# Performance work log

Hardware: AMD Instinct MI355X
Metric: run time of the kernel (lower is better)

The kernel has to match this reference:

```python
import jax, jax.numpy as jnp
import numpy as np

NUM_GROUP = 512
GROUP_SIZE = 32


def setup_inputs() -> dict:
    key = jax.random.key(0)
    pts = jax.random.normal(key, (8, 8192, 6), dtype=jnp.float32)
    return {"pts": pts}


def _fps(xyz, num_group):
    """Farthest point sampling. xyz: (B, N, 3) -> indices (B, G)."""
    B, N, _ = xyz.shape

    def body(carry, _):
        dist, far = carry  # dist: (B, N) running min sq-dist to chosen set; far: (B,)
        centroid = jnp.take_along_axis(xyz, far[:, None, None], axis=1)  # (B, 1, 3)
        d = jnp.sum((xyz - centroid) ** 2, axis=-1)  # (B, N)
        dist = jnp.minimum(dist, d)
        new_far = jnp.argmax(dist, axis=-1)  # (B,)
        return (dist, new_far), far

    init = (jnp.full((B, N), 1e10, dtype=xyz.dtype), jnp.zeros((B,), dtype=jnp.int32))
    _, idxs = jax.lax.scan(body, init, None, length=num_group)  # (G, B)
    return idxs.T  # (B, G)


def _knn(k, xyz, center):
    """k nearest neighbors of each center among xyz. Returns idx (B, G, k)."""
    # squared distances (B, G, N)
    d2 = (jnp.sum(center ** 2, -1)[:, :, None]
          + jnp.sum(xyz ** 2, -1)[:, None, :]
          - 2.0 * jnp.einsum('bgc,bnc->bgn', center, xyz))
    _, idx = jax.lax.top_k(-d2, k)
    return idx


def reference(pts):
    xyz = pts[:, :, :3].astype(jnp.float32)
    fps_idx = _fps(xyz, NUM_GROUP)  # (B, G)
    center = jnp.take_along_axis(xyz, fps_idx[:, :, None], axis=1)  # (B, G, 3)
    idx = _knn(GROUP_SIZE, xyz, center)  # (B, G, K)
    # gather neighborhoods per batch: pts (B, N, C), idx (B, G, K) -> (B, G, K, C)
    neighborhood = jax.vmap(lambda p, i: p[i])(pts, idx)
    # center only the xyz channels
    nb_xyz = neighborhood[..., :3] - center[:, :, None, :]
    neighborhood = jnp.concatenate([nb_xyz, neighborhood[..., 3:]], axis=-1)
    return (neighborhood, center)
```

## Files before the change

### kernel.cpp

```cpp
#include <hip/hip_runtime.h>
#include <stdint.h>

#define BATCH 8
#define NPTS 8192
#define NGRP 512
#define KNN 32
#define NCH 6

#define FPS_T 256
#define FPS_PPT (NPTS / FPS_T)
#define PAIRS (FPS_PPT / 2)
#define FPS_NW (FPS_T / 64)

#define NBLK 248
#define KNN_WAVES ((NBLK - BATCH) * FPS_NW)

typedef float f2 __attribute__((ext_vector_type(2)));

__device__ __forceinline__ f2 pk_add(f2 a, f2 b) {
    f2 d;
    asm("v_pk_add_f32 %0, %1, %2" : "=v"(d) : "v"(a), "v"(b));
    return d;
}
__device__ __forceinline__ f2 pk_mul(f2 a, f2 b) {
    f2 d;
    asm("v_pk_mul_f32 %0, %1, %2" : "=v"(d) : "v"(a), "v"(b));
    return d;
}

template <int CTRL>
__device__ __forceinline__ unsigned long long dpp_max64(unsigned long long k) {
    int lo = (int)(unsigned)k;
    int hi = (int)(unsigned)(k >> 32);
    int plo = __builtin_amdgcn_update_dpp(lo, lo, CTRL, 0xF, 0xF, false);
    int phi = __builtin_amdgcn_update_dpp(hi, hi, CTRL, 0xF, 0xF, false);
    unsigned long long o =
        ((unsigned long long)(unsigned)phi << 32) | (unsigned)plo;
    return (o > k) ? o : k;
}

__device__ __forceinline__ unsigned long long knn_key(const float* __restrict__ base,
                                                      int p, float cx, float cy,
                                                      float cz, float cc) {
    float x = base[p * NCH + 0];
    float y = base[p * NCH + 1];
    float z = base[p * NCH + 2];
    float xx = __fadd_rn(__fadd_rn(__fmul_rn(x, x), __fmul_rn(y, y)), __fmul_rn(z, z));
    float dt = fmaf(cz, z, fmaf(cy, y, __fmul_rn(cx, x)));
    float d2 = __fsub_rn(__fadd_rn(cc, xx), __fmul_rn(2.0f, dt));
    unsigned int bits = __float_as_uint(d2);
    unsigned int ord = bits ^ ((unsigned)((int)bits >> 31) | 0x80000000u);
    return ((unsigned long long)ord << 13) | (unsigned)p;
}

__global__ __launch_bounds__(FPS_T) void fused_kernel(const float* __restrict__ pts,
                                                      float* __restrict__ out_ctr,
                                                      float* __restrict__ out_nb,
                                                      unsigned int* __restrict__ faridx,
                                                      int fstride) {
    __shared__ float xs[NPTS], ys[NPTS], zs[NPTS];
    __shared__ float ctr_lds[NGRP * 3];
    __shared__ unsigned long long slots[2][FPS_NW];

    const int tid = threadIdx.x;

    if (blockIdx.x < BATCH) {
        const int b = blockIdx.x;
        const float* base = pts + (size_t)b * NPTS * NCH;

        f2 x2[PAIRS], y2[PAIRS], z2[PAIRS], dist2[PAIRS];
#pragma unroll
        for (int i = 0; i < PAIRS; ++i) {
            int p0 = tid + (2 * i) * FPS_T;
            int p1 = tid + (2 * i + 1) * FPS_T;
            float xa = base[p0 * NCH + 0], ya = base[p0 * NCH + 1], za = base[p0 * NCH + 2];
            float xb = base[p1 * NCH + 0], yb = base[p1 * NCH + 1], zb = base[p1 * NCH + 2];
            x2[i] = (f2){xa, xb};
            y2[i] = (f2){ya, yb};
            z2[i] = (f2){za, zb};
            dist2[i] = (f2){1e10f, 1e10f};
            xs[p0] = xa; ys[p0] = ya; zs[p0] = za;
            xs[p1] = xb; ys[p1] = yb; zs[p1] = zb;
        }
        __syncthreads();

        int far = 0;
        const int wid  = tid >> 6;
        const int lane = tid & 63;

        for (int g = 0; g < NGRP; ++g) {
            float cx = xs[far], cy = ys[far], cz = zs[far];
            if (tid == 0) {
                ctr_lds[g * 3 + 0] = cx;
                ctr_lds[g * 3 + 1] = cy;
                ctr_lds[g * 3 + 2] = cz;
                __hip_atomic_store(&faridx[(b * NGRP + g) * fstride], (unsigned)far,
                                   __ATOMIC_RELAXED, __HIP_MEMORY_SCOPE_AGENT);
            }
            if (g == NGRP - 1) break;

            f2 ncx = (f2){-cx, -cx};
            f2 ncy = (f2){-cy, -cy};
            f2 ncz = (f2){-cz, -cz};

            float bestv = -1.0f;
            int bestj = 0;
#pragma unroll
            for (int i = 0; i < PAIRS; ++i) {
                f2 dx = pk_add(x2[i], ncx);
                f2 dy = pk_add(y2[i], ncy);
                f2 dz = pk_add(z2[i], ncz);
                f2 sx = pk_mul(dx, dx);
                f2 sy = pk_mul(dy, dy);
                f2 t  = pk_add(sx, sy);
                f2 sz = pk_mul(dz, dz);
                f2 d  = pk_add(t, sz);
                float nd0 = fminf(dist2[i].x, d.x);
                float nd1 = fminf(dist2[i].y, d.y);
                dist2[i].x = nd0;
                dist2[i].y = nd1;
                if (nd0 > bestv) { bestv = nd0; bestj = 2 * i; }
                if (nd1 > bestv) { bestv = nd1; bestj = 2 * i + 1; }
            }
            int bestp = tid + bestj * FPS_T;
            unsigned long long key =
                ((unsigned long long)__float_as_uint(bestv) << 13) |
                (unsigned)(8191 - bestp);

            key = dpp_max64<0x111>(key);
            key = dpp_max64<0x112>(key);
            key = dpp_max64<0x114>(key);
            key = dpp_max64<0x118>(key);
            key = dpp_max64<0x142>(key);
            key = dpp_max64<0x143>(key);
            if (lane == 63) slots[g & 1][wid] = key;
            __syncthreads();

            unsigned long long best = slots[g & 1][0];
#pragma unroll
            for (int w = 1; w < FPS_NW; ++w) {
                unsigned long long o = slots[g & 1][w];
                best = (o > best) ? o : best;
            }
            far = 8191 - (int)(best & 8191ULL);
        }

        __syncthreads();
        float* ctr = out_ctr + (size_t)b * NGRP * 3;
        for (int i = tid; i < NGRP * 3; i += FPS_T) ctr[i] = ctr_lds[i];

    } else {
        const int wid  = tid >> 6;
        const int lane = tid & 63;
        const int W = (blockIdx.x - BATCH) * FPS_NW + wid;

        for (int e = W; e < BATCH * NGRP; e += KNN_WAVES) {
            const int g  = e >> 3;
            const int b  = e & 7;
            const int bg = b * NGRP + g;
            const float* base = pts + (size_t)b * NPTS * NCH;

            unsigned fidx;
            if (lane == 0) {
                while ((fidx = __hip_atomic_load(&faridx[bg * fstride],
                                                 __ATOMIC_RELAXED,
                                                 __HIP_MEMORY_SCOPE_AGENT)) == 0xFFFFFFFFu)
                    __builtin_amdgcn_s_sleep(8);
            }
            fidx = (unsigned)__shfl((int)fidx, 0, 64);

            const float cx = base[fidx * NCH + 0];
            const float cy = base[fidx * NCH + 1];
            const float cz = base[fidx * NCH + 2];
            const float cc = __fadd_rn(__fadd_rn(__fmul_rn(cx, cx), __fmul_rn(cy, cy)),
                                       __fmul_rn(cz, cz));

            unsigned long long R = knn_key(base, lane, cx, cy, cz, cc);
#pragma unroll
            for (int k = 2; k <= 64; k <<= 1) {
#pragma unroll
                for (int j = k >> 1; j > 0; j >>= 1) {
                    unsigned long long o = __shfl_xor(R, j, 64);
                    bool takeMin = (((lane & k) == 0) == ((lane & j) == 0));
                    unsigned long long mn = (o < R) ? o : R;
                    unsigned long long mx = (o < R) ? R : o;
                    R = takeMin ? mn : mx;
                }
            }
            unsigned long long R31 = __shfl(R, 31, 64);

            for (int c = 1; c < NPTS / 64; ++c) {
                unsigned long long key = knn_key(base, c * 64 + lane, cx, cy, cz, cc);
                unsigned long long qual = __ballot(key < R31);
                while (qual) {
                    int src = __ffsll(qual) - 1;
                    qual &= qual - 1;
                    unsigned long long bk = __shfl(key, src, 64);
                    int rank = __popcll(__ballot(R < bk));
                    unsigned long long Rp = __shfl_up(R, 1, 64);
                    R = (lane == rank) ? bk : ((lane > rank) ? Rp : R);
                    R31 = __shfl(R, 31, 64);
                }
            }

            if (lane < KNN) {
                int idx = (int)(R & 8191ULL);
                const float* s = base + (size_t)idx * NCH;
                float* d = out_nb + ((size_t)bg * KNN + lane) * NCH;
                d[0] = s[0] - cx;
                d[1] = s[1] - cy;
                d[2] = s[2] - cz;
                d[3] = s[3];
                d[4] = s[4];
                d[5] = s[5];
            }
        }
    }
}

extern "C" void kernel_launch(void* const* d_in, const int* in_sizes, int n_in,
                              void* d_out, int out_size, void* d_ws, size_t ws_size,
                              hipStream_t stream) {
    const float* pts = (const float*)d_in[0];
    float* out = (float*)d_out;
    float* out_nb  = out;
    float* out_ctr = out + (size_t)BATCH * NGRP * KNN * NCH;

    const size_t nctr = (size_t)BATCH * NGRP;
    int fstride = (ws_size >= nctr * 16 * sizeof(unsigned)) ? 16 : 1;
    unsigned int* faridx = (unsigned int*)d_ws;

    hipMemsetAsync(d_ws, 0xFF, nctr * (size_t)fstride * sizeof(unsigned), stream);
    hipLaunchKernelGGL(fused_kernel, dim3(NBLK), dim3(FPS_T), 0, stream,
                       pts, out_ctr, out_nb, faridx, fstride);
}
```

Baseline: 513.2 us.

## Run FPS iterations on a small candidate set in one wave, lazily folding centers

Farthest point sampling now collects, after each full pass, the points whose running min distance is at least 80% (or 95%) of the current maximum into a shared candidate list of up to 512. Wave 0 alone then runs further FPS steps on just those candidates, with no block barriers. It keeps going while the best candidate distance stays above the threshold, since any point outside the list is provably below it. Later, all threads fold the skipped centers into their full per-point distances in one batched pass, cutting the per-iteration block sync and full 8192-point reductions. The cost is extra rebuild passes, LDS atomics for compaction, and more tricky control flow that must match the reference's argmax tie-breaking exactly.

```diff
diff --git a/kernel.cpp b/kernel.cpp
--- a/kernel.cpp
+++ b/kernel.cpp
@@ -14,8 +14,11 @@
 
 #define NBLK 248
 #define KNN_WAVES ((NBLK - BATCH) * FPS_NW)
+#define NCAND 512
+#define DONE_TAG 0xFFFFFFFFu
 
 typedef float f2 __attribute__((ext_vector_type(2)));
+typedef float f4 __attribute__((ext_vector_type(4)));
 
 __device__ __forceinline__ f2 pk_add(f2 a, f2 b) {
     f2 d;
@@ -26,6 +29,11 @@
     f2 d;
     asm("v_pk_mul_f32 %0, %1, %2" : "=v"(d) : "v"(a), "v"(b));
     return d;
+}
+
+__device__ __forceinline__ unsigned long long max64(unsigned long long a,
+                                                    unsigned long long b) {
+    return (a > b) ? a : b;
 }
 
 template <int CTRL>
@@ -36,7 +44,29 @@
     int phi = __builtin_amdgcn_update_dpp(hi, hi, CTRL, 0xF, 0xF, false);
     unsigned long long o =
         ((unsigned long long)(unsigned)phi << 32) | (unsigned)plo;
-    return (o > k) ? o : k;
+    return max64(o, k);
+}
+
+__device__ __forceinline__ unsigned long long wave_max_dir(unsigned long long k) {
+    k = dpp_max64<0x111>(k);
+    k = dpp_max64<0x112>(k);
+    k = dpp_max64<0x114>(k);
+    k = dpp_max64<0x118>(k);
+    k = dpp_max64<0x142>(k);
+    k = dpp_max64<0x143>(k);
+    return k;
+}
+
+__device__ __forceinline__ unsigned long long wave_max_all(unsigned long long k) {
+    k = dpp_max64<0xB1>(k);
+    k = dpp_max64<0x4E>(k);
+    k = dpp_max64<0x141>(k);
+    k = dpp_max64<0x140>(k);
+    unsigned long long o = __shfl_xor(k, 16, 64);
+    k = max64(k, o);
+    o = __shfl_xor(k, 32, 64);
+    k = max64(k, o);
+    return k;
 }
 
 __device__ __forceinline__ unsigned long long knn_key(const float* __restrict__ base,
@@ -53,14 +83,18 @@
     return ((unsigned long long)ord << 13) | (unsigned)p;
 }
 
-__global__ __launch_bounds__(FPS_T) void fused_kernel(const float* __restrict__ pts,
-                                                      float* __restrict__ out_ctr,
-                                                      float* __restrict__ out_nb,
-                                                      unsigned int* __restrict__ faridx,
-                                                      int fstride) {
+__global__ __launch_bounds__(FPS_T, 1) void fused_kernel(const float* __restrict__ pts,
+                                                         float* __restrict__ out_ctr,
+                                                         float* __restrict__ out_nb,
+                                                         unsigned int* __restrict__ faridx,
+                                                         int fstride) {
     __shared__ float xs[NPTS], ys[NPTS], zs[NPTS];
     __shared__ float ctr_lds[NGRP * 3];
-    __shared__ unsigned long long slots[2][FPS_NW];
+    __shared__ unsigned long long slots[FPS_NW];
+    __shared__ f4 candP[NCAND];
+    __shared__ float cvA[NCAND];
+    __shared__ unsigned ctl_gshared;
+    __shared__ int ctl_count;
 
     const int tid = threadIdx.x;
 
@@ -84,68 +118,171 @@
         }
         __syncthreads();
 
-        int far = 0;
         const int wid  = tid >> 6;
         const int lane = tid & 63;
 
-        for (int g = 0; g < NGRP; ++g) {
-            float cx = xs[far], cy = ys[far], cz = zs[far];
-            if (tid == 0) {
-                ctr_lds[g * 3 + 0] = cx;
-                ctr_lds[g * 3 + 1] = cy;
-                ctr_lds[g * 3 + 2] = cz;
-                __hip_atomic_store(&faridx[(b * NGRP + g) * fstride], (unsigned)far,
-                                   __ATOMIC_RELAXED, __HIP_MEMORY_SCOPE_AGENT);
-            }
-            if (g == NGRP - 1) break;
-
-            f2 ncx = (f2){-cx, -cx};
-            f2 ncy = (f2){-cy, -cy};
-            f2 ncz = (f2){-cz, -cz};
-
-            float bestv = -1.0f;
-            int bestj = 0;
-#pragma unroll
-            for (int i = 0; i < PAIRS; ++i) {
-                f2 dx = pk_add(x2[i], ncx);
-                f2 dy = pk_add(y2[i], ncy);
-                f2 dz = pk_add(z2[i], ncz);
-                f2 sx = pk_mul(dx, dx);
-                f2 sy = pk_mul(dy, dy);
-                f2 t  = pk_add(sx, sy);
-                f2 sz = pk_mul(dz, dz);
-                f2 d  = pk_add(t, sz);
-                float nd0 = fminf(dist2[i].x, d.x);
-                float nd1 = fminf(dist2[i].y, d.y);
-                dist2[i].x = nd0;
-                dist2[i].y = nd1;
-                if (nd0 > bestv) { bestv = nd0; bestj = 2 * i; }
-                if (nd1 > bestv) { bestv = nd1; bestj = 2 * i + 1; }
-            }
-            int bestp = tid + bestj * FPS_T;
-            unsigned long long key =
-                ((unsigned long long)__float_as_uint(bestv) << 13) |
-                (unsigned)(8191 - bestp);
-
-            key = dpp_max64<0x111>(key);
-            key = dpp_max64<0x112>(key);
-            key = dpp_max64<0x114>(key);
-            key = dpp_max64<0x118>(key);
-            key = dpp_max64<0x142>(key);
-            key = dpp_max64<0x143>(key);
-            if (lane == 63) slots[g & 1][wid] = key;
+        int far = 0, g = 0, lastFold = 0, cnt = 0;
+        bool valid = false;
+        float vb = 0.0f;
+
+        while (true) {
+            if (wid == 0) {
+                while (true) {
+                    float ccx = xs[far], ccy = ys[far], ccz = zs[far];
+                    if (lane == 0) {
+                        ctr_lds[g * 3 + 0] = ccx;
+                        ctr_lds[g * 3 + 1] = ccy;
+                        ctr_lds[g * 3 + 2] = ccz;
+                        __hip_atomic_store(&faridx[(b * NGRP + g) * fstride],
+                                           (unsigned)far, __ATOMIC_RELAXED,
+                                           __HIP_MEMORY_SCOPE_AGENT);
+                    }
+                    if (g == NGRP - 1) {
+                        if (lane == 0) ctl_gshared = DONE_TAG;
+                        break;
+                    }
+                    if (!valid) {
+                        if (lane == 0) ctl_gshared = (unsigned)g;
+                        break;
+                    }
+                    unsigned long long wkey = 0;
+#pragma unroll
+                    for (int s = 0; s < NCAND / 64; ++s) {
+                        int i = lane + s * 64;
+                        if (i < cnt) {
+                            f4 P = candP[i];
+                            float pv = cvA[i];
+                            float dx = __fsub_rn(P.x, ccx);
+                            float dy = __fsub_rn(P.y, ccy);
+                            float dz = __fsub_rn(P.z, ccz);
+                            float d = __fadd_rn(__fadd_rn(__fmul_rn(dx, dx),
+                                                          __fmul_rn(dy, dy)),
+                                                __fmul_rn(dz, dz));
+                            float nv = fminf(pv, d);
+                            cvA[i] = nv;
+                            unsigned idx = __float_as_uint(P.w);
+                            unsigned long long k =
+                                ((unsigned long long)__float_as_uint(nv) << 13) |
+                                (unsigned)(8191 - idx);
+                            wkey = max64(wkey, k);
+                        }
+                    }
+                    wkey = wave_max_all(wkey);
+                    float wv = __uint_as_float((unsigned)(wkey >> 13));
+                    if (!(wv > vb)) {
+                        if (lane == 0) ctl_gshared = (unsigned)g;
+                        break;
+                    }
+                    far = 8191 - (int)(wkey & 0x1FFFULL);
+                    ++g;
+                }
+            }
             __syncthreads();
-
-            unsigned long long best = slots[g & 1][0];
-#pragma unroll
-            for (int w = 1; w < FPS_NW; ++w) {
-                unsigned long long o = slots[g & 1][w];
-                best = (o > best) ? o : best;
-            }
-            far = 8191 - (int)(best & 8191ULL);
+            unsigned gr = ctl_gshared;
+            if (gr == DONE_TAG) break;
+            if (tid == 0) ctl_count = 0;
+
+            for (int h = lastFold; h < (int)gr; ++h) {
+                float ccx = ctr_lds[h * 3 + 0];
+                float ccy = ctr_lds[h * 3 + 1];
+                float ccz = ctr_lds[h * 3 + 2];
+                f2 ncx = (f2){-ccx, -ccx};
+                f2 ncy = (f2){-ccy, -ccy};
+                f2 ncz = (f2){-ccz, -ccz};
+#pragma unroll
+                for (int i = 0; i < PAIRS; ++i) {
+                    f2 dx = pk_add(x2[i], ncx);
+                    f2 dy = pk_add(y2[i], ncy);
+                    f2 dz = pk_add(z2[i], ncz);
+                    f2 sx = pk_mul(dx, dx);
+                    f2 sy = pk_mul(dy, dy);
+                    f2 t  = pk_add(sx, sy);
+                    f2 sz = pk_mul(dz, dz);
+                    f2 d  = pk_add(t, sz);
+                    dist2[i].x = fminf(dist2[i].x, d.x);
+                    dist2[i].y = fminf(dist2[i].y, d.y);
+                }
+            }
+
+            {
+                float ccx = ctr_lds[gr * 3 + 0];
+                float ccy = ctr_lds[gr * 3 + 1];
+                float ccz = ctr_lds[gr * 3 + 2];
+                f2 ncx = (f2){-ccx, -ccx};
+                f2 ncy = (f2){-ccy, -ccy};
+                f2 ncz = (f2){-ccz, -ccz};
+                float bestv = -1.0f;
+                int bestj = 0;
+#pragma unroll
+                for (int i = 0; i < PAIRS; ++i) {
+                    f2 dx = pk_add(x2[i], ncx);
+                    f2 dy = pk_add(y2[i], ncy);
+                    f2 dz = pk_add(z2[i], ncz);
+                    f2 sx = pk_mul(dx, dx);
+                    f2 sy = pk_mul(dy, dy);
+                    f2 t  = pk_add(sx, sy);
+                    f2 sz = pk_mul(dz, dz);
+                    f2 d  = pk_add(t, sz);
+                    float nd0 = fminf(dist2[i].x, d.x);
+                    float nd1 = fminf(dist2[i].y, d.y);
+                    dist2[i].x = nd0;
+                    dist2[i].y = nd1;
+                    if (nd0 > bestv) { bestv = nd0; bestj = 2 * i; }
+                    if (nd1 > bestv) { bestv = nd1; bestj = 2 * i + 1; }
+                }
+                int bestp = tid + bestj * FPS_T;
+                unsigned long long key =
+                    ((unsigned long long)__float_as_uint(bestv) << 13) |
+                    (unsigned)(8191 - bestp);
+                key = wave_max_dir(key);
+                if (lane == 63) slots[wid] = key;
+            }
+            __syncthreads();
+
+            unsigned long long m01 = max64(slots[0], slots[1]);
+            unsigned long long m23 = max64(slots[2], slots[3]);
+            unsigned long long best = max64(m01, m23);
+            far = 8191 - (int)(best & 0x1FFFULL);
+            float M = __uint_as_float((unsigned)(best >> 13));
+
+            float vbTry = __fmul_rn(0.80f, M);
+            for (int attempt = 0; attempt < 2; ++attempt) {
+#pragma unroll
+                for (int i = 0; i < PAIRS; ++i) {
+                    float v0 = dist2[i].x, v1 = dist2[i].y;
+                    if (v0 >= vbTry) {
+                        int pos = atomicAdd(&ctl_count, 1);
+                        if (pos < NCAND) {
+                            candP[pos] = (f4){x2[i].x, y2[i].x, z2[i].x,
+                                              __uint_as_float((unsigned)(tid + (2 * i) * FPS_T))};
+                            cvA[pos] = v0;
+                        }
+                    }
+                    if (v1 >= vbTry) {
+                        int pos = atomicAdd(&ctl_count, 1);
+                        if (pos < NCAND) {
+                            candP[pos] = (f4){x2[i].y, y2[i].y, z2[i].y,
+                                              __uint_as_float((unsigned)(tid + (2 * i + 1) * FPS_T))};
+                            cvA[pos] = v1;
+                        }
+                    }
+                }
+                __syncthreads();
+                int c = ctl_count;
+                if (c <= NCAND) { valid = true; cnt = c; vb = vbTry; break; }
+                if (attempt == 0) {
+                    if (tid == 0) ctl_count = 0;
+                    vbTry = __fmul_rn(0.95f, M);
+                    __syncthreads();
+                } else {
+                    valid = false;
+                }
+            }
+
+            g = (int)gr + 1;
+            lastFold = (int)gr + 1;
         }
 
-        __syncthreads();
         float* ctr = out_ctr + (size_t)b * NGRP * 3;
         for (int i = tid; i < NGRP * 3; i += FPS_T) ctr[i] = ctr_lds[i];
 
```

Measured after the change: 667.4 us (median of 3 runs). 1.3x slower.

## Split FPS argmax into four chains and reduce via LDS atomicMax

Applied to the files above, without the earlier changes.

The per-thread argmax in the farthest point sampling loop now keeps four independent running maxima instead of one, which shortens the serial dependency chain. The cross-lane reduction is cut to two quad-level DPP steps, after which every fourth lane does an LDS 64-bit atomicMax into a double-buffered slot. The old full-wave DPP reduction and per-wave slot scan are gone. The cost is 64 atomics per block per iteration contending on one LDS address, plus an extra reset of the alternate slot each iteration.

```diff
diff --git a/kernel.cpp b/kernel.cpp
--- a/kernel.cpp
+++ b/kernel.cpp
@@ -26,6 +26,11 @@
     f2 d;
     asm("v_pk_mul_f32 %0, %1, %2" : "=v"(d) : "v"(a), "v"(b));
     return d;
+}
+
+__device__ __forceinline__ unsigned long long max64(unsigned long long a,
+                                                    unsigned long long b) {
+    return (a > b) ? a : b;
 }
 
 template <int CTRL>
@@ -36,7 +41,7 @@
     int phi = __builtin_amdgcn_update_dpp(hi, hi, CTRL, 0xF, 0xF, false);
     unsigned long long o =
         ((unsigned long long)(unsigned)phi << 32) | (unsigned)plo;
-    return (o > k) ? o : k;
+    return max64(o, k);
 }
 
 __device__ __forceinline__ unsigned long long knn_key(const float* __restrict__ base,
@@ -60,7 +65,7 @@
                                                       int fstride) {
     __shared__ float xs[NPTS], ys[NPTS], zs[NPTS];
     __shared__ float ctr_lds[NGRP * 3];
-    __shared__ unsigned long long slots[2][FPS_NW];
+    __shared__ unsigned long long bslot[2];
 
     const int tid = threadIdx.x;
 
@@ -82,10 +87,10 @@
             xs[p0] = xa; ys[p0] = ya; zs[p0] = za;
             xs[p1] = xb; ys[p1] = yb; zs[p1] = zb;
         }
+        if (tid == 0) { bslot[0] = 0ULL; bslot[1] = 0ULL; }
         __syncthreads();
 
         int far = 0;
-        const int wid  = tid >> 6;
         const int lane = tid & 63;
 
         for (int g = 0; g < NGRP; ++g) {
@@ -96,6 +101,7 @@
                 ctr_lds[g * 3 + 2] = cz;
                 __hip_atomic_store(&faridx[(b * NGRP + g) * fstride], (unsigned)far,
                                    __ATOMIC_RELAXED, __HIP_MEMORY_SCOPE_AGENT);
+                bslot[(g + 1) & 1] = 0ULL;
             }
             if (g == NGRP - 1) break;
 
@@ -103,8 +109,8 @@
             f2 ncy = (f2){-cy, -cy};
             f2 ncz = (f2){-cz, -cz};
 
-            float bestv = -1.0f;
-            int bestj = 0;
+            float v0 = -1.0f, v1 = -1.0f, v2v = -1.0f, v3 = -1.0f;
+            int j0 = 0, j1 = 0, j2 = 0, j3 = 0;
 #pragma unroll
             for (int i = 0; i < PAIRS; ++i) {
                 f2 dx = pk_add(x2[i], ncx);
@@ -119,30 +125,35 @@
                 float nd1 = fminf(dist2[i].y, d.y);
                 dist2[i].x = nd0;
                 dist2[i].y = nd1;
-                if (nd0 > bestv) { bestv = nd0; bestj = 2 * i; }
-                if (nd1 > bestv) { bestv = nd1; bestj = 2 * i + 1; }
-            }
-            int bestp = tid + bestj * FPS_T;
-            unsigned long long key =
-                ((unsigned long long)__float_as_uint(bestv) << 13) |
-                (unsigned)(8191 - bestp);
-
-            key = dpp_max64<0x111>(key);
-            key = dpp_max64<0x112>(key);
-            key = dpp_max64<0x114>(key);
-            key = dpp_max64<0x118>(key);
-            key = dpp_max64<0x142>(key);
-            key = dpp_max64<0x143>(key);
-            if (lane == 63) slots[g & 1][wid] = key;
+                if (i & 1) {
+                    if (nd0 > v2v) { v2v = nd0; j2 = 2 * i; }
+                    if (nd1 > v3)  { v3  = nd1; j3 = 2 * i + 1; }
+                } else {
+                    if (nd0 > v0)  { v0  = nd0; j0 = 2 * i; }
+                    if (nd1 > v1)  { v1  = nd1; j1 = 2 * i + 1; }
+                }
+            }
+
+            unsigned long long k0 =
+                ((unsigned long long)__float_as_uint(v0) << 13) |
+                (unsigned)(8191 - (tid + j0 * FPS_T));
+            unsigned long long k1 =
+                ((unsigned long long)__float_as_uint(v1) << 13) |
+                (unsigned)(8191 - (tid + j1 * FPS_T));
+            unsigned long long k2 =
+                ((unsigned long long)__float_as_uint(v2v) << 13) |
+                (unsigned)(8191 - (tid + j2 * FPS_T));
+            unsigned long long k3 =
+                ((unsigned long long)__float_as_uint(v3) << 13) |
+                (unsigned)(8191 - (tid + j3 * FPS_T));
+            unsigned long long k = max64(max64(k0, k1), max64(k2, k3));
+
+            k = dpp_max64<0xB1>(k);
+            k = dpp_max64<0x4E>(k);
+            if ((lane & 3) == 0) atomicMax(&bslot[g & 1], k);
             __syncthreads();
 
-            unsigned long long best = slots[g & 1][0];
-#pragma unroll
-            for (int w = 1; w < FPS_NW; ++w) {
-                unsigned long long o = slots[g & 1][w];
-                best = (o > best) ? o : best;
-            }
-            far = 8191 - (int)(best & 8191ULL);
+            far = 8191 - (int)(bslot[g & 1] & 0x1FFFULL);
         }
 
         __syncthreads();
```

Result: slower. 847.2 us (+65.1%).
